# Performance work log

Measured on AMD Instinct MI355X. Metric: run time of the kernel, lower is better.

## Reference

```python
import jax, jax.numpy as jnp
import numpy as np

B, S, D, V = 2, 256, 512, 32000
W_WIN, GAMMA = 20, 2.0
MEM_LEN, NUM_MEM, K_SIM, K_CONT = 16, 256, 8, 4


def _modularity(sim, bnd):
    deg = sim.sum(1)
    tot = deg.sum()
    com = jnp.cumsum(bnd).astype(jnp.int32)
    exp = deg[:, None] * deg[None, :] / (tot + 1e-10)
    mask = (com[:, None] == com[None, :]).astype(sim.dtype)
    return ((sim - exp) * mask).sum() / (tot + 1e-10)


def _conductance(sim, bnd):
    n = sim.shape[0]
    deg = sim.sum(1)
    tot = deg.sum()
    com = jnp.cumsum(bnd).astype(jnp.int32)
    oh = jax.nn.one_hot(com, n + 1, dtype=sim.dtype)  # [N, N+1] fixed class count (empty communities contribute 0)
    vol = oh.T @ deg
    inter = oh.T @ sim @ oh
    inter = inter * (1.0 - jnp.eye(n + 1, dtype=sim.dtype))
    cuts = inter.sum(1)
    minv = jnp.minimum(vol, tot - vol)
    cond = cuts / (minv + 1e-10)
    # torch averages over num_communities = max(com)+1
    return cond.sum() / (com[-1].astype(sim.dtype) + 1.0)


def _forward(query, key, value, attention_mask, target_tokens, brain_w,
             storage_w1, storage_b1, storage_w2, storage_b2, sim_w, sim_b,
             memory_keys, memory_values, memory_lengths, memory_timestamps):
    # --- surprise: per-token NLL of target under brain logits ---
    logits = jnp.einsum('bsd,vd->bsv', query, brain_w)
    logp = jax.nn.log_softmax(logits, axis=-1)
    surprise = -jnp.take_along_axis(logp, target_tokens[..., None], axis=-1)[..., 0]  # [B,S]
    # --- dynamic threshold over sliding windows (unbiased std, as torch) ---
    widx = jnp.arange(S - W_WIN + 1)[:, None] + jnp.arange(W_WIN)[None, :]
    win = surprise[:, widx]  # [B, S-W+1, W]
    thr = win.mean(-1) + GAMMA * jnp.std(win, axis=-1, ddof=1)
    thr = jnp.concatenate([jnp.repeat(thr[:, :1], W_WIN - 1, axis=1), thr], axis=1)
    boundaries = (surprise > thr).astype(query.dtype)  # [B,S]
    # --- refine boundaries via modularity / conductance on token similarity graph ---
    sims = jnp.einsum('bnd,bmd->bnm', query, query)
    curQ = jax.vmap(_modularity)(sims, boundaries)
    curC = jax.vmap(_conductance)(sims, boundaries)
    b_idx = jnp.repeat(jnp.arange(B), S)
    t_idx = jnp.tile(jnp.arange(S), B)

    def cand(b, t):  # evaluate removing boundary at (b,t)
        tb = boundaries[b].at[t].set(0.0)
        return _modularity(sims[b], tb), _conductance(sims[b], tb)

    newQ, newC = jax.vmap(cand)(b_idx, t_idx)
    impr = ((newQ > curQ[b_idx]) | (newC < curC[b_idx])).reshape(B, S)
    refined = jnp.where((boundaries > 0) & impr, 0.0, boundaries)
    # --- event segmentation: labels via cumsum; position-in-event via cummax of segment starts ---
    labels = jnp.cumsum(refined, axis=1).astype(jnp.int32)  # [B,S] in [0,S]
    t_r = jnp.arange(S)
    changed = jnp.concatenate([jnp.ones((B, 1), bool), labels[:, 1:] != labels[:, :-1]], axis=1)
    start = jax.lax.cummax(jnp.where(changed, t_r[None, :], 0), axis=1)
    pos = t_r[None, :] - start  # [B,S] position within event
    bflat = jnp.repeat(jnp.arange(B), S)
    lflat = labels.reshape(-1)
    pflat = pos.reshape(-1)  # tokens with pos >= MEM_LEN are truncated (OOB -> dropped)
    events = jnp.zeros((B, S + 1, MEM_LEN, D), query.dtype)
    events = events.at[bflat, lflat, pflat].add(query.reshape(-1, D), mode='drop')
    counts = jnp.zeros((B, S + 1), jnp.int32).at[bflat, lflat].add(1)
    # --- pack non-empty events into circular memory bank (memory_index = 0, timestamp = 0) ---
    flat_ev = events.reshape(B * (S + 1), MEM_LEN, D)
    flat_ct = counts.reshape(-1)
    nonempty = flat_ct > 0
    rank = jnp.cumsum(nonempty) - 1
    slot = jnp.where(nonempty, rank % NUM_MEM, NUM_MEM)  # OOB slot -> dropped
    mem_keys = memory_keys.at[slot].set(flat_ev[:, 0, :], mode='drop')
    mem_vals = memory_values.at[slot].set(flat_ev, mode='drop')
    mem_lens = memory_lengths.at[slot].set(jnp.minimum(flat_ct, MEM_LEN).astype(memory_lengths.dtype), mode='drop')
    mem_ts = memory_timestamps.at[slot].set(jnp.zeros(slot.shape, memory_timestamps.dtype), mode='drop')
    # --- retrieval: kNN over memory keys with projected mean query ---
    qm = (jnp.einsum('bsd,ed->bse', query, sim_w) + sim_b).mean(1)  # [B,D]
    scores = qm @ mem_keys.T  # [B, NUM_MEM]
    valid = mem_lens > 0
    scores = jnp.where(valid[None, :], scores, -1e9)
    _, top_i = jax.lax.top_k(scores, K_SIM)
    sim_buf = mem_vals[top_i].reshape(B, K_SIM * MEM_LEN, D)
    rec = jnp.where(valid, jnp.arange(NUM_MEM), -1)  # contiguity = most recently written slots
    _, cont_i = jax.lax.top_k(rec, K_CONT)
    cont_buf = jnp.broadcast_to(mem_vals[cont_i].reshape(1, K_CONT * MEM_LEN, D), (B, K_CONT * MEM_LEN, D))
    storage = lambda x: jax.nn.relu(x @ storage_w1.T + storage_b1) @ storage_w2.T + storage_b2
    context = jnp.concatenate([storage(sim_buf), storage(cont_buf), key], axis=1)  # [B, 192+S, D]
    mem_total = (K_SIM + K_CONT) * MEM_LEN
    ext_mask = jnp.concatenate([jnp.ones((B, mem_total), attention_mask.dtype), attention_mask], axis=1)
    return query, context, context, ext_mask


def setup_inputs():
    rng = jax.random.key(0)
    ks = jax.random.split(rng, 10)
    sc = 0.02
    return {
        'query': jax.random.normal(ks[0], (B, S, D), jnp.float32),
        'key': jax.random.normal(ks[1], (B, S, D), jnp.float32),
        'value': jax.random.normal(ks[2], (B, S, D), jnp.float32),
        'attention_mask': jnp.ones((B, S), jnp.float32),
        'target_tokens': jax.random.randint(ks[3], (B, S), 0, V),
        'brain_w': jax.random.normal(ks[4], (V, D), jnp.float32) * sc,
        'storage_w1': jax.random.normal(ks[5], (D, D), jnp.float32) * sc,
        'storage_b1': jnp.zeros((D,), jnp.float32),
        'storage_w2': jax.random.normal(ks[6], (D, D), jnp.float32) * sc,
        'storage_b2': jnp.zeros((D,), jnp.float32),
        'sim_w': jax.random.normal(ks[7], (D, D), jnp.float32) * sc,
        'sim_b': jnp.zeros((D,), jnp.float32),
        'memory_keys': jnp.zeros((NUM_MEM, D), jnp.float32),
        'memory_values': jnp.zeros((NUM_MEM, MEM_LEN, D), jnp.float32),
        'memory_lengths': jnp.zeros((NUM_MEM,), jnp.int32),
        'memory_timestamps': jnp.zeros((NUM_MEM,), jnp.float32),
    }


def reference(query, key, value, attention_mask, target_tokens, brain_w, storage_w1, storage_b1, storage_w2, storage_b2, sim_w, sim_b, memory_keys, memory_values, memory_lengths, memory_timestamps):
    return _forward(query, key, value, attention_mask, target_tokens, brain_w, storage_w1, storage_b1, storage_w2, storage_b2, sim_w, sim_b, memory_keys, memory_values, memory_lengths, memory_timestamps)
```

## Files before the change

kernel.cpp:

```cpp
#include <hip/hip_runtime.h>

constexpr int Bb = 2;
constexpr int Ss = 256;
constexpr int Dd = 512;
constexpr int Vv = 32000;
constexpr int NVB = Vv / 64;
constexpr float GAMMA_C = 2.0f;
constexpr int MEMLEN = 16;
constexpr int NMEM = 256;
constexpr int MTOT = (8 + 4) * MEMLEN;
constexpr int CTXROWS = MTOT + Ss;

constexpr size_t NQ   = (size_t)Bb * Ss * Dd;
constexpr size_t OC1  = NQ;
constexpr size_t NCTX = (size_t)Bb * CTXROWS * Dd;
constexpr size_t OC2  = OC1 + NCTX;
constexpr size_t OMASK = OC2 + NCTX;

constexpr size_t WS_FLOATS_NEEDED = 256000 + 512 + 512 + 131072 + 131584 + 512 +
                                    1024 + 1024 + 512 + 196608 + 196608 + 4096;

__device__ __forceinline__ void gemm64x64_k512(const float* __restrict__ A,
                                               const float* __restrict__ Bm,
                                               float acc[4][4],
                                               float4* __restrict__ Qs4,
                                               float4* __restrict__ Ws4) {
  const int t = threadIdx.x;
  const int tn = t & 15, tm = t >> 4;
  float* __restrict__ Qf = (float*)Qs4;
  float* __restrict__ Wf = (float*)Ws4;
  #pragma unroll 2
  for (int kc = 0; kc < 512; kc += 32) {
    #pragma unroll
    for (int e = 0; e < 2; ++e) {
      const int idx4 = t + 256 * e;
      const int m = idx4 >> 3;
      const int kg = idx4 & 7;
      const float4 qa = *(const float4*)(A + (size_t)m * 512 + kc + kg * 4);
      const float4 wb = *(const float4*)(Bm + (size_t)m * 512 + kc + kg * 4);
      const int fb = ((kg * 4) * 16 + ((m >> 2) ^ kg)) * 4 + (m & 3);
      Qf[fb]       = qa.x; Qf[fb + 64]  = qa.y;
      Qf[fb + 128] = qa.z; Qf[fb + 192] = qa.w;
      Wf[fb]       = wb.x; Wf[fb + 64]  = wb.y;
      Wf[fb + 128] = wb.z; Wf[fb + 192] = wb.w;
    }
    __syncthreads();
    #pragma unroll
    for (int k = 0; k < 32; ++k) {
      const int swz = (k >> 2) & 7;
      const float4 a4 = Qs4[k * 16 + (tm ^ swz)];
      const float4 b4 = Ws4[k * 16 + (tn ^ swz)];
      const float av[4] = {a4.x, a4.y, a4.z, a4.w};
      const float bv[4] = {b4.x, b4.y, b4.z, b4.w};
      #pragma unroll
      for (int i = 0; i < 4; ++i)
        #pragma unroll
        for (int j = 0; j < 4; ++j)
          acc[i][j] += av[i] * bv[j];
    }
    __syncthreads();
  }
}

__global__ __launch_bounds__(256) void k_logits(const float* __restrict__ q,
                                                const float* __restrict__ bw,
                                                float* __restrict__ partial) {
  __shared__ float4 As4[512];
  __shared__ float4 Bs4[1024];
  __shared__ float red[64 * 17];
  const int bv = blockIdx.x;
  const int bm = blockIdx.y;
  const int t = threadIdx.x;
  const int tn = t & 15, tm = t >> 4;
  const float* A  = q  + (size_t)bm * 64 * 512;
  const float* Bm = bw + (size_t)bv * 128 * 512;
  float* Af = (float*)As4;
  float* Bf = (float*)Bs4;
  float acc0[4][4] = {};
  float acc1[4][4] = {};
  #pragma unroll 1
  for (int kc = 0; kc < 512; kc += 32) {
    #pragma unroll
    for (int e = 0; e < 2; ++e) {
      const int idx = t + 256 * e;
      const int m = idx >> 3, kg = idx & 7;
      const float4 v = *(const float4*)(A + (size_t)m * 512 + kc + kg * 4);
      const int fb = ((kg * 4) * 16 + ((m >> 2) ^ kg)) * 4 + (m & 3);
      Af[fb] = v.x; Af[fb + 64] = v.y; Af[fb + 128] = v.z; Af[fb + 192] = v.w;
    }
    #pragma unroll
    for (int e = 0; e < 4; ++e) {
      const int idx = t + 256 * e;
      const int mB = idx >> 3, kg = idx & 7;
      const float4 v = *(const float4*)(Bm + (size_t)mB * 512 + kc + kg * 4);
      const int m4 = mB >> 2;
      const int g = (m4 & 24) | ((m4 & 7) ^ kg);
      const int fb = ((kg * 4) * 32 + g) * 4 + (mB & 3);
      Bf[fb] = v.x; Bf[fb + 128] = v.y; Bf[fb + 256] = v.z; Bf[fb + 384] = v.w;
    }
    __syncthreads();
    #pragma unroll
    for (int k = 0; k < 32; ++k) {
      const int swz = (k >> 2) & 7;
      const float4 a4 = As4[k * 16 + (tm ^ swz)];
      const int g0 = (tn & 8) | ((tn & 7) ^ swz);
      const float4 b0 = Bs4[k * 32 + g0];
      const float4 b1 = Bs4[k * 32 + 16 + g0];
      const float av[4]  = {a4.x, a4.y, a4.z, a4.w};
      const float b0v[4] = {b0.x, b0.y, b0.z, b0.w};
      const float b1v[4] = {b1.x, b1.y, b1.z, b1.w};
      #pragma unroll
      for (int i = 0; i < 4; ++i)
        #pragma unroll
        for (int j = 0; j < 4; ++j) {
          acc0[i][j] += av[i] * b0v[j];
          acc1[i][j] += av[i] * b1v[j];
        }
    }
    __syncthreads();
  }
  #pragma unroll
  for (int i = 0; i < 4; ++i) {
    float s = 0.f;
    #pragma unroll
    for (int j = 0; j < 4; ++j) s += expf(acc0[i][j]);
    red[(tm * 4 + i) * 17 + tn] = s;
  }
  __syncthreads();
  if (t < 64) {
    float s = 0.f;
    #pragma unroll
    for (int j = 0; j < 16; ++j) s += red[t * 17 + j];
    partial[(size_t)(bv * 2) * 512 + bm * 64 + t] = s;
  }
  __syncthreads();
  #pragma unroll
  for (int i = 0; i < 4; ++i) {
    float s = 0.f;
    #pragma unroll
    for (int j = 0; j < 4; ++j) s += expf(acc1[i][j]);
    red[(tm * 4 + i) * 17 + tn] = s;
  }
  __syncthreads();
  if (t < 64) {
    float s = 0.f;
    #pragma unroll
    for (int j = 0; j < 16; ++j) s += red[t * 17 + j];
    partial[(size_t)(bv * 2 + 1) * 512 + bm * 64 + t] = s;
  }
}

constexpr int MISC_SIMS = 32;
constexpr int MISC_QBAR = MISC_SIMS + 4;
constexpr int MISC_LSE  = MISC_QBAR + 16;
constexpr int MISC_NBLK = MISC_LSE + 2052;

__global__ __launch_bounds__(256) void k_misc(const float* __restrict__ q,
                                              const float* __restrict__ key,
                                              const float* __restrict__ amask,
                                              const float* __restrict__ partial,
                                              float* __restrict__ sims,
                                              float* __restrict__ qbar,
                                              double* __restrict__ pc,
                                              float* __restrict__ out) {
  __shared__ float4 sh4[1024];
  const int bx = blockIdx.x, t = threadIdx.x;
  if (bx < MISC_SIMS) {
    int b = bx >> 4, rem = bx & 15;
    int m0 = (rem >> 2) * 64, n0 = (rem & 3) * 64;
    float acc[4][4] = {};
    const float* qb = q + (size_t)b * Ss * Dd;
    gemm64x64_k512(qb + (size_t)m0 * 512, qb + (size_t)n0 * 512, acc, sh4, sh4 + 512);
    int tn = t & 15, tm = t >> 4;
    float* outp = sims + (size_t)b * Ss * Ss;
    #pragma unroll
    for (int i = 0; i < 4; ++i) {
      float4 v = make_float4(acc[i][0], acc[i][1], acc[i][2], acc[i][3]);
      *(float4*)&outp[(size_t)(m0 + tm * 4 + i) * 256 + n0 + tn * 4] = v;
    }
  } else if (bx < MISC_QBAR) {
    int id = (bx - MISC_SIMS) * 256 + t;
    int b = id >> 9, d = id & 511;
    float s = 0.f;
    for (int ss2 = 0; ss2 < 256; ++ss2) s += q[((size_t)(b * 256 + ss2)) * 512 + d];
    qbar[id] = s * (1.0f / 256.0f);
  } else if (bx < MISC_LSE) {
    int idx = bx - MISC_QBAR;
    int c = idx >> 1, rb = idx & 1;
    int r = rb * 256 + t;
    int j0 = c * 63, j1 = (j0 + 63 < NVB) ? j0 + 63 : NVB;
    double s = 0.0;
    for (int j = j0; j < j1; ++j) s += (double)partial[(size_t)j * 512 + r];
    pc[c * 512 + r] = s;
  } else {
    int id = (bx - MISC_LSE) * 256 + t;
    if (id < 262144) { out[id] = q[id]; return; }
    if (id < 524288) {
      int id2 = id - 262144;
      int b = id2 >> 17;
      int s = (id2 >> 9) & 255;
      int d = id2 & 511;
      float v = key[id2];
      size_t p = OC1 + ((size_t)(b * 448 + 192 + s)) * 512 + d;
      out[p] = v;
      out[p + NCTX] = v;
      return;
    }
    if (id < 525184) {
      int j = id - 524288;
      int b = j / 448, c = j - b * 448;
      out[OMASK + j] = (c < 192) ? 1.0f : amask[b * 256 + (c - 192)];
    }
  }
}

__global__ __launch_bounds__(256) void k_sur(const float* __restrict__ q,
                                             const float* __restrict__ bw,
                                             const int* __restrict__ tgt,
                                             const double* __restrict__ pc,
                                             float* __restrict__ sur) {
  int wid = blockIdx.x * 4 + (threadIdx.x >> 6);
  int lane = threadIdx.x & 63;
  int tg = tgt[wid];
  const float* qp = q + (size_t)wid * 512;
  const float* wp = bw + (size_t)tg * 512;
  float a = 0.f;
  #pragma unroll
  for (int j = 0; j < 8; ++j) a += qp[lane + 64 * j] * wp[lane + 64 * j];
  #pragma unroll
  for (int off = 32; off; off >>= 1) a += __shfl_xor(a, off);
  if (lane == 0) {
    double s = 0.0;
    #pragma unroll
    for (int c = 0; c < 8; ++c) s += pc[c * 512 + wid];
    float lsef = (float)log(s);
    sur[wid] = lsef - a;
  }
}

__global__ __launch_bounds__(256) void k_bound(const float* __restrict__ sur,
                                               int* __restrict__ bnd) {
  __shared__ float ss[256];
  __shared__ float thrw[237];
  int b = blockIdx.x, t = threadIdx.x;
  ss[t] = sur[b * 256 + t];
  __syncthreads();
  if (t < 237) {
    float mn = 0.f;
    #pragma unroll
    for (int e = 0; e < 20; ++e) mn += ss[t + e];
    mn *= (1.0f / 20.0f);
    float v = 0.f;
    #pragma unroll
    for (int e = 0; e < 20; ++e) { float d = ss[t + e] - mn; v += d * d; }
    thrw[t] = mn + GAMMA_C * sqrtf(v * (1.0f / 19.0f));
  }
  __syncthreads();
  float th = (t <= 18) ? thrw[0] : thrw[t - 19];
  bnd[b * 256 + t] = (ss[t] > th) ? 1 : 0;
}

__global__ __launch_bounds__(256) void k_rowpref(const float* __restrict__ sims,
                                                 float* __restrict__ R,
                                                 float* __restrict__ deg) {
  int wid = blockIdx.x * 4 + (threadIdx.x >> 6);
  int lane = threadIdx.x & 63;
  int b = wid >> 8, i = wid & 255;
  const float* row = sims + (size_t)b * 65536 + (size_t)i * 256;
  float4 v = *(const float4*)&row[lane * 4];
  float c0 = v.x, c1 = c0 + v.y, c2 = c1 + v.z, c3 = c2 + v.w;
  float ls = c3;
  float sc = ls;
  for (int off = 1; off < 64; off <<= 1) {
    float u = __shfl_up(sc, off);
    if (lane >= off) sc += u;
  }
  float ex = sc - ls;
  float* Rr = R + (size_t)b * (256 * 257) + (size_t)i * 257;
  Rr[lane * 4 + 1] = ex + c0;
  Rr[lane * 4 + 2] = ex + c1;
  Rr[lane * 4 + 3] = ex + c2;
  Rr[lane * 4 + 4] = ex + c3;
  if (lane == 0) Rr[0] = 0.f;
  if (lane == 63) deg[b * 256 + i] = ex + c3;
}

__global__ __launch_bounds__(256) void k_refine(const int* __restrict__ bnd,
                                                const float* __restrict__ R,
                                                const float* __restrict__ deg,
                                                int* __restrict__ nseg,
                                                int* __restrict__ segstart_o,
                                                int* __restrict__ segcnt_o) {
  __shared__ int sb[256], lab[256];
  __shared__ int segst[258];
  __shared__ float Dc[257], Sc[257], Cr[257];
  __shared__ float degsh[256];
  __shared__ float Stm[256], Ctm[256];
  __shared__ float sh[6];
  int b = blockIdx.x, t = threadIdx.x;
  sb[t] = bnd[b * 256 + t];
  degsh[t] = deg[b * 256 + t];
  for (int c = t; c < 258; c += 256) segst[c] = -1;
  __syncthreads();
  int a = 0;
  for (int i = 0; i <= t; ++i) a += sb[i];
  lab[t] = a;
  __syncthreads();
  if (t == 0 || lab[t - 1] != lab[t]) segst[lab[t]] = t;
  __syncthreads();
  int nb = lab[255];
  const float* Rb = R + (size_t)b * (256 * 257);
  {
    int c = lab[t];
    int a1 = segst[c];
    int e1 = (c == nb) ? 255 : (segst[c + 1] - 1);
    const float* Rrow = Rb + (size_t)t * 257;
    Stm[t] = Rrow[e1 + 1] - Rrow[a1];
    float cv = 0.f;
    if (c < nb) {
      int a2 = segst[c + 1];
      int e2 = (c + 1 == nb) ? 255 : (segst[c + 2] - 1);
      cv = Rrow[e2 + 1] - Rrow[a2];
    }
    Ctm[t] = cv;
  }
  __syncthreads();
  for (int c = t; c <= nb; c += 256) {
    float Dv = 0.f, Sv = 0.f, Cv = 0.f;
    int a1 = segst[c];
    if (a1 >= 0) {
      int e1 = (c == nb) ? 255 : (segst[c + 1] - 1);
      for (int i = a1; i <= e1; ++i) { Dv += degsh[i]; Sv += Stm[i]; Cv += Ctm[i]; }
    }
    Dc[c] = Dv; Sc[c] = Sv; Cr[c] = Cv;
  }
  __syncthreads();
  if (t == 0) {
    float tot = 0.f;
    for (int i = 0; i < 256; ++i) tot += degsh[i];
    float tote = tot + 1e-10f;
    float Qun = 0.f, Cs = 0.f;
    for (int c = 0; c <= nb; ++c) {
      Qun += Sc[c] - Dc[c] * Dc[c] / tote;
      Cs  += (Dc[c] - Sc[c]) / (fminf(Dc[c], tot - Dc[c]) + 1e-10f);
    }
    sh[0] = tot; sh[1] = tote; sh[2] = Qun; sh[3] = Cs;
    sh[4] = Qun / tote; sh[5] = Cs / (float)(nb + 1);
  }
  __syncthreads();
  int r = sb[t];
  if (r == 1) {
    float tot = sh[0], tote = sh[1], Qun = sh[2], Cs = sh[3], curQ = sh[4], curC = sh[5];
    int c2 = lab[t], c1 = c2 - 1;
    if (segst[c1] < 0) {
      float newC0 = Cs / (float)nb;
      if (newC0 < curC) r = 0;
    } else {
      float D1 = Dc[c1], S1 = Sc[c1], D2 = Dc[c2], S2 = Sc[c2];
      float Dm = D1 + D2, Sm = S1 + S2 + 2.0f * Cr[c1];
      float tq1 = S1 - D1 * D1 / tote;
      float tq2 = S2 - D2 * D2 / tote;
      float tqm = Sm - Dm * Dm / tote;
      float newQ = (Qun - tq1 - tq2 + tqm) / tote;
      float tc1 = (D1 - S1) / (fminf(D1, tot - D1) + 1e-10f);
      float tc2 = (D2 - S2) / (fminf(D2, tot - D2) + 1e-10f);
      float tcm = (Dm - Sm) / (fminf(Dm, tot - Dm) + 1e-10f);
      float newC = (Cs - tc1 - tc2 + tcm) / (float)nb;
      if (newQ > curQ || newC < curC) r = 0;
    }
  }
  __syncthreads();
  sb[t] = r;
  __syncthreads();
  if (t == 0) {
    int ns = 0, st = 0;
    for (int i = 1; i <= 256; ++i) {
      if (i == 256 || sb[i] == 1) {
        segstart_o[b * 257 + ns] = st;
        segcnt_o[b * 257 + ns] = i - st;
        ns++;
        st = i;
      }
    }
    nseg[b] = ns;
  }
}

__global__ __launch_bounds__(256) void k_slots(const int* __restrict__ nseg,
                                               const int* __restrict__ segstart_i,
                                               const int* __restrict__ segcnt_i,
                                               const int* __restrict__ meml_in,
                                               int* __restrict__ slot_b,
                                               int* __restrict__ slot_start,
                                               int* __restrict__ slot_cnt,
                                               int* __restrict__ cont) {
  __shared__ unsigned char validsh[256];
  __shared__ int ns01[2];
  int t = threadIdx.x;
  if (t < 2) ns01[t] = nseg[t];
  __syncthreads();
  int ns0 = ns01[0], total = ns0 + ns01[1];
  int rank = -1;
  for (int r = t; r < total; r += 256) rank = r;
  int bb = 0, st = 0, ct = 0;
  if (rank >= 0) {
    bb = (rank >= ns0) ? 1 : 0;
    int s = rank - bb * ns0;
    st = segstart_i[bb * 257 + s];
    ct = segcnt_i[bb * 257 + s];
  }
  slot_b[t] = bb; slot_start[t] = st; slot_cnt[t] = ct;
  validsh[t] = (ct > 0 || meml_in[t] > 0) ? 1 : 0;
  __syncthreads();
  if (t == 0) {
    int k = 0;
    for (int n = 255; n >= 0 && k < 4; --n) if (validsh[n]) cont[k++] = n;
    for (int n = 0; n < 256 && k < 4; ++n) if (!validsh[n]) cont[k++] = n;
  }
}

__global__ __launch_bounds__(256) void k_qm(const float* __restrict__ qbar,
                                            const float* __restrict__ simw,
                                            const float* __restrict__ simb,
                                            float* __restrict__ qm) {
  int wid = blockIdx.x * 4 + (threadIdx.x >> 6);
  int lane = threadIdx.x & 63;
  int b = wid >> 9, e = wid & 511;
  float a = 0.f;
  #pragma unroll
  for (int j = 0; j < 8; ++j)
    a += qbar[b * 512 + lane + 64 * j] * simw[(size_t)e * 512 + lane + 64 * j];
  #pragma unroll
  for (int off = 32; off; off >>= 1) a += __shfl_xor(a, off);
  if (lane == 0) qm[b * 512 + e] = a + simb[e];
}

__global__ __launch_bounds__(256) void k_scores(const float* __restrict__ q,
                                                const float* __restrict__ memk,
                                                const int* __restrict__ meml,
                                                const int* __restrict__ slot_b,
                                                const int* __restrict__ slot_start,
                                                const int* __restrict__ slot_cnt,
                                                const float* __restrict__ qm,
                                                float* __restrict__ scores) {
  int wid = blockIdx.x * 4 + (threadIdx.x >> 6);
  int lane = threadIdx.x & 63;
  int b = wid >> 8, n = wid & 255;
  const float* kp = nullptr;
  if (slot_cnt[n] > 0) kp = q + ((size_t)(slot_b[n] * 256 + slot_start[n])) * 512;
  else if (meml[n] > 0) kp = memk + (size_t)n * 512;
  float a = 0.f;
  if (kp) {
    #pragma unroll
    for (int j = 0; j < 8; ++j) a += qm[b * 512 + lane + 64 * j] * kp[lane + 64 * j];
    #pragma unroll
    for (int off = 32; off; off >>= 1) a += __shfl_xor(a, off);
  }
  if (lane == 0) scores[b * 256 + n] = kp ? a : -1000000000.0f;
}

__global__ __launch_bounds__(64) void k_topk(const float* __restrict__ scores,
                                             int* __restrict__ topi) {
  int b = blockIdx.x, lane = threadIdx.x;
  float v[4];
  #pragma unroll
  for (int j = 0; j < 4; ++j) v[j] = scores[b * 256 + lane * 4 + j];
  int chosen = 0;
  for (int k = 0; k < 8; ++k) {
    float best = -3.4e38f; int bi = 0x7fffffff;
    #pragma unroll
    for (int j = 0; j < 4; ++j) {
      if (!(chosen & (1 << j))) {
        float s = v[j]; int n = lane * 4 + j;
        if (s > best || (s == best && n < bi)) { best = s; bi = n; }
      }
    }
    #pragma unroll
    for (int off = 32; off; off >>= 1) {
      float ob = __shfl_xor(best, off);
      int oi = __shfl_xor(bi, off);
      if (ob > best || (ob == best && oi < bi)) { best = ob; bi = oi; }
    }
    if ((bi >> 2) == lane) chosen |= 1 << (bi & 3);
    if (lane == 0) topi[b * 8 + k] = bi;
  }
}

__global__ __launch_bounds__(256) void k_gather(const float* __restrict__ q,
                                                const float* __restrict__ memv,
                                                const int* __restrict__ topi,
                                                const int* __restrict__ cont,
                                                const int* __restrict__ slot_b,
                                                const int* __restrict__ slot_start,
                                                const int* __restrict__ slot_cnt,
                                                float* __restrict__ xg) {
  int id = blockIdx.x * 256 + threadIdx.x;
  int d = id & 511;
  int rb = id >> 9;
  int b = rb / 192;
  int r = rb - b * 192;
  int p = r & 15;
  int slot = (r < 128) ? topi[b * 8 + (r >> 4)] : cont[(r - 128) >> 4];
  float val;
  int cnt = slot_cnt[slot];
  if (cnt > 0) {
    int ml = cnt < 16 ? cnt : 16;
    val = (p < ml) ? q[((size_t)(slot_b[slot] * 256 + slot_start[slot] + p)) * 512 + d] : 0.f;
  } else {
    val = memv[((size_t)slot * 16 + p) * 512 + d];
  }
  xg[id] = val;
}

__global__ __launch_bounds__(256) void k_mlp1(const float* __restrict__ xg,
                                              const float* __restrict__ w1,
                                              const float* __restrict__ b1,
                                              float* __restrict__ h) {
  __shared__ float4 Qs4[512];
  __shared__ float4 Ws4[512];
  int n0 = blockIdx.x * 64, m0 = blockIdx.y * 64;
  float acc[4][4] = {};
  gemm64x64_k512(xg + (size_t)m0 * 512, w1 + (size_t)n0 * 512, acc, Qs4, Ws4);
  int t = threadIdx.x, tn = t & 15, tm = t >> 4;
  #pragma unroll
  for (int i = 0; i < 4; ++i) {
    int m = m0 + tm * 4 + i;
    #pragma unroll
    for (int j = 0; j < 4; ++j) {
      int n = n0 + tn * 4 + j;
      h[(size_t)m * 512 + n] = fmaxf(acc[i][j] + b1[n], 0.f);
    }
  }
}

__global__ __launch_bounds__(256) void k_mlp2(const float* __restrict__ h,
                                              const float* __restrict__ w2,
                                              const float* __restrict__ b2,
                                              float* __restrict__ out) {
  __shared__ float4 Qs4[512];
  __shared__ float4 Ws4[512];
  int n0 = blockIdx.x * 64, m0 = blockIdx.y * 64;
  float acc[4][4] = {};
  gemm64x64_k512(h + (size_t)m0 * 512, w2 + (size_t)n0 * 512, acc, Qs4, Ws4);
  int t = threadIdx.x, tn = t & 15, tm = t >> 4;
  #pragma unroll
  for (int i = 0; i < 4; ++i) {
    int m = m0 + tm * 4 + i;
    int b = (m >= 192) ? 1 : 0;
    int rr = m - b * 192;
    int n = n0 + tn * 4;
    float4 v = make_float4(acc[i][0] + b2[n], acc[i][1] + b2[n + 1],
                           acc[i][2] + b2[n + 2], acc[i][3] + b2[n + 3]);
    size_t base = OC1 + ((size_t)(b * 448 + rr)) * 512 + n;
    *(float4*)&out[base] = v;
    *(float4*)&out[base + NCTX] = v;
  }
}

extern "C" void kernel_launch(void* const* d_in, const int* in_sizes, int n_in,
                              void* d_out, int out_size, void* d_ws, size_t ws_size,
                              hipStream_t stream) {
  if (ws_size < WS_FLOATS_NEEDED * sizeof(float)) return;

  const float* q     = (const float*)d_in[0];
  const float* key   = (const float*)d_in[1];
  const float* amask = (const float*)d_in[3];
  const int*   tgt   = (const int*)d_in[4];
  const float* bw    = (const float*)d_in[5];
  const float* w1    = (const float*)d_in[6];
  const float* b1    = (const float*)d_in[7];
  const float* w2    = (const float*)d_in[8];
  const float* b2    = (const float*)d_in[9];
  const float* simw  = (const float*)d_in[10];
  const float* simb  = (const float*)d_in[11];
  const float* memk  = (const float*)d_in[12];
  const float* memv  = (const float*)d_in[13];
  const int*   meml  = (const int*)d_in[14];
  float* out = (float*)d_out;

  float* w = (float*)d_ws;
  float* p_partial = w;
  float* p_lse    = p_partial + 256000;
  float* p_sur    = p_lse + 512;
  float* p_sims   = p_sur + 512;
  float* p_R      = p_sims + 131072;
  float* p_deg    = p_R + 131584;
  float* p_qbar   = p_deg + 512;
  float* p_qm     = p_qbar + 1024;
  float* p_scores = p_qm + 1024;
  float* p_xg     = p_scores + 512;
  float* p_h      = p_xg + 196608;
  double* p_pc    = (double*)p_h;
  int* ip         = (int*)(p_h + 196608);
  int* ip_bnd     = ip;
  int* ip_nseg    = ip + 512;
  int* ip_segst   = ip + 514;
  int* ip_segcnt  = ip + 1028;
  int* ip_slotb   = ip + 1542;
  int* ip_slotst  = ip + 1798;
  int* ip_slotcnt = ip + 2054;
  int* ip_topi    = ip + 2310;
  int* ip_cont    = ip + 2326;

  k_logits<<<dim3(250, 8), 256, 0, stream>>>(q, bw, p_partial);
  k_misc<<<MISC_NBLK, 256, 0, stream>>>(q, key, amask, p_partial,
                                        p_sims, p_qbar, p_pc, out);
  k_sur<<<128, 256, 0, stream>>>(q, bw, tgt, p_pc, p_sur);
  k_bound<<<2, 256, 0, stream>>>(p_sur, ip_bnd);
  k_rowpref<<<128, 256, 0, stream>>>(p_sims, p_R, p_deg);
  k_refine<<<2, 256, 0, stream>>>(ip_bnd, p_R, p_deg, ip_nseg, ip_segst, ip_segcnt);
  k_slots<<<1, 256, 0, stream>>>(ip_nseg, ip_segst, ip_segcnt, meml,
                                 ip_slotb, ip_slotst, ip_slotcnt, ip_cont);
  k_qm<<<256, 256, 0, stream>>>(p_qbar, simw, simb, p_qm);
  k_scores<<<128, 256, 0, stream>>>(q, memk, meml, ip_slotb, ip_slotst, ip_slotcnt,
                                    p_qm, p_scores);
  k_topk<<<2, 64, 0, stream>>>(p_scores, ip_topi);
  k_gather<<<768, 256, 0, stream>>>(q, memv, ip_topi, ip_cont,
                                    ip_slotb, ip_slotst, ip_slotcnt, p_xg);
  k_mlp1<<<dim3(8, 6), 256, 0, stream>>>(p_xg, w1, b1, p_h);
  k_mlp2<<<dim3(8, 6), 256, 0, stream>>>(p_h, w2, b2, out);
}
```

Before: 485.0 us.

## Fuse pipeline kernels to cut launch count from thirteen to seven

Merges the logits GEMM with the sims/qbar/copy work into one launch and merges the LSE partial reduction, row prefix sums and qm projection into a second. Boundary detection, refinement and slot assignment are folded into a single 512-thread block. Top-k selection and the row gather are folded into the first MLP GEMM, which now reads its rows through pointers. The aim is to remove launch gaps and intermediate round trips, at the cost of heavier per-block branching and a single-block serial stage.

```diff
diff --git a/kernel.cpp b/kernel.cpp
--- a/kernel.cpp
+++ b/kernel.cpp
@@ -19,6 +19,11 @@
 
 constexpr size_t WS_FLOATS_NEEDED = 256000 + 512 + 512 + 131072 + 131584 + 512 +
                                     1024 + 1024 + 512 + 196608 + 196608 + 4096;
+
+constexpr int K1_LOGITS = 2000;
+constexpr int K1_SIMS   = K1_LOGITS + 32;
+constexpr int K1_QBAR   = K1_SIMS + 4;
+constexpr int K1_NBLK   = K1_QBAR + 2052;
 
 __device__ __forceinline__ void gemm64x64_k512(const float* __restrict__ A,
                                                const float* __restrict__ Bm,
@@ -62,155 +67,191 @@
   }
 }
 
-__global__ __launch_bounds__(256) void k_logits(const float* __restrict__ q,
-                                                const float* __restrict__ bw,
-                                                float* __restrict__ partial) {
-  __shared__ float4 As4[512];
-  __shared__ float4 Bs4[1024];
-  __shared__ float red[64 * 17];
-  const int bv = blockIdx.x;
-  const int bm = blockIdx.y;
-  const int t = threadIdx.x;
-  const int tn = t & 15, tm = t >> 4;
-  const float* A  = q  + (size_t)bm * 64 * 512;
-  const float* Bm = bw + (size_t)bv * 128 * 512;
-  float* Af = (float*)As4;
-  float* Bf = (float*)Bs4;
-  float acc0[4][4] = {};
-  float acc1[4][4] = {};
-  #pragma unroll 1
-  for (int kc = 0; kc < 512; kc += 32) {
-    #pragma unroll
-    for (int e = 0; e < 2; ++e) {
-      const int idx = t + 256 * e;
-      const int m = idx >> 3, kg = idx & 7;
-      const float4 v = *(const float4*)(A + (size_t)m * 512 + kc + kg * 4);
-      const int fb = ((kg * 4) * 16 + ((m >> 2) ^ kg)) * 4 + (m & 3);
-      Af[fb] = v.x; Af[fb + 64] = v.y; Af[fb + 128] = v.z; Af[fb + 192] = v.w;
-    }
-    #pragma unroll
-    for (int e = 0; e < 4; ++e) {
-      const int idx = t + 256 * e;
-      const int mB = idx >> 3, kg = idx & 7;
-      const float4 v = *(const float4*)(Bm + (size_t)mB * 512 + kc + kg * 4);
-      const int m4 = mB >> 2;
-      const int g = (m4 & 24) | ((m4 & 7) ^ kg);
-      const int fb = ((kg * 4) * 32 + g) * 4 + (mB & 3);
-      Bf[fb] = v.x; Bf[fb + 128] = v.y; Bf[fb + 256] = v.z; Bf[fb + 384] = v.w;
-    }
-    __syncthreads();
-    #pragma unroll
-    for (int k = 0; k < 32; ++k) {
-      const int swz = (k >> 2) & 7;
-      const float4 a4 = As4[k * 16 + (tm ^ swz)];
-      const int g0 = (tn & 8) | ((tn & 7) ^ swz);
-      const float4 b0 = Bs4[k * 32 + g0];
-      const float4 b1 = Bs4[k * 32 + 16 + g0];
-      const float av[4]  = {a4.x, a4.y, a4.z, a4.w};
-      const float b0v[4] = {b0.x, b0.y, b0.z, b0.w};
-      const float b1v[4] = {b1.x, b1.y, b1.z, b1.w};
-      #pragma unroll
-      for (int i = 0; i < 4; ++i)
-        #pragma unroll
-        for (int j = 0; j < 4; ++j) {
-          acc0[i][j] += av[i] * b0v[j];
-          acc1[i][j] += av[i] * b1v[j];
-        }
-    }
-    __syncthreads();
-  }
-  #pragma unroll
-  for (int i = 0; i < 4; ++i) {
-    float s = 0.f;
-    #pragma unroll
-    for (int j = 0; j < 4; ++j) s += expf(acc0[i][j]);
-    red[(tm * 4 + i) * 17 + tn] = s;
-  }
-  __syncthreads();
-  if (t < 64) {
-    float s = 0.f;
-    #pragma unroll
-    for (int j = 0; j < 16; ++j) s += red[t * 17 + j];
-    partial[(size_t)(bv * 2) * 512 + bm * 64 + t] = s;
-  }
-  __syncthreads();
-  #pragma unroll
-  for (int i = 0; i < 4; ++i) {
-    float s = 0.f;
-    #pragma unroll
-    for (int j = 0; j < 4; ++j) s += expf(acc1[i][j]);
-    red[(tm * 4 + i) * 17 + tn] = s;
-  }
-  __syncthreads();
-  if (t < 64) {
-    float s = 0.f;
-    #pragma unroll
-    for (int j = 0; j < 16; ++j) s += red[t * 17 + j];
-    partial[(size_t)(bv * 2 + 1) * 512 + bm * 64 + t] = s;
-  }
-}
-
-constexpr int MISC_SIMS = 32;
-constexpr int MISC_QBAR = MISC_SIMS + 4;
-constexpr int MISC_LSE  = MISC_QBAR + 16;
-constexpr int MISC_NBLK = MISC_LSE + 2052;
-
-__global__ __launch_bounds__(256) void k_misc(const float* __restrict__ q,
+__global__ __launch_bounds__(256) void k_main(const float* __restrict__ q,
+                                              const float* __restrict__ bw,
                                               const float* __restrict__ key,
                                               const float* __restrict__ amask,
-                                              const float* __restrict__ partial,
+                                              float* __restrict__ partial,
                                               float* __restrict__ sims,
                                               float* __restrict__ qbar,
-                                              double* __restrict__ pc,
                                               float* __restrict__ out) {
-  __shared__ float4 sh4[1024];
-  const int bx = blockIdx.x, t = threadIdx.x;
-  if (bx < MISC_SIMS) {
-    int b = bx >> 4, rem = bx & 15;
+  __shared__ __align__(16) char smem[28928];
+  const int b = blockIdx.x, t = threadIdx.x;
+  if (b < K1_LOGITS) {
+    float4* As4 = (float4*)smem;
+    float4* Bs4 = As4 + 512;
+    float* red  = (float*)(Bs4 + 1024);
+    const int bv = b >> 3;
+    const int bm = b & 7;
+    const int tn = t & 15, tm = t >> 4;
+    const float* A  = q  + (size_t)bm * 64 * 512;
+    const float* Bm = bw + (size_t)bv * 128 * 512;
+    float* Af = (float*)As4;
+    float* Bf = (float*)Bs4;
+    float acc0[4][4] = {};
+    float acc1[4][4] = {};
+    #pragma unroll 1
+    for (int kc = 0; kc < 512; kc += 32) {
+      #pragma unroll
+      for (int e = 0; e < 2; ++e) {
+        const int idx = t + 256 * e;
+        const int m = idx >> 3, kg = idx & 7;
+        const float4 v = *(const float4*)(A + (size_t)m * 512 + kc + kg * 4);
+        const int fb = ((kg * 4) * 16 + ((m >> 2) ^ kg)) * 4 + (m & 3);
+        Af[fb] = v.x; Af[fb + 64] = v.y; Af[fb + 128] = v.z; Af[fb + 192] = v.w;
+      }
+      #pragma unroll
+      for (int e = 0; e < 4; ++e) {
+        const int idx = t + 256 * e;
+        const int mB = idx >> 3, kg = idx & 7;
+        const float4 v = *(const float4*)(Bm + (size_t)mB * 512 + kc + kg * 4);
+        const int m4 = mB >> 2;
+        const int g = (m4 & 24) | ((m4 & 7) ^ kg);
+        const int fb = ((kg * 4) * 32 + g) * 4 + (mB & 3);
+        Bf[fb] = v.x; Bf[fb + 128] = v.y; Bf[fb + 256] = v.z; Bf[fb + 384] = v.w;
+      }
+      __syncthreads();
+      #pragma unroll
+      for (int k = 0; k < 32; ++k) {
+        const int swz = (k >> 2) & 7;
+        const float4 a4 = As4[k * 16 + (tm ^ swz)];
+        const int g0 = (tn & 8) | ((tn & 7) ^ swz);
+        const float4 b0 = Bs4[k * 32 + g0];
+        const float4 b1 = Bs4[k * 32 + 16 + g0];
+        const float av[4]  = {a4.x, a4.y, a4.z, a4.w};
+        const float b0v[4] = {b0.x, b0.y, b0.z, b0.w};
+        const float b1v[4] = {b1.x, b1.y, b1.z, b1.w};
+        #pragma unroll
+        for (int i = 0; i < 4; ++i)
+          #pragma unroll
+          for (int j = 0; j < 4; ++j) {
+            acc0[i][j] += av[i] * b0v[j];
+            acc1[i][j] += av[i] * b1v[j];
+          }
+      }
+      __syncthreads();
+    }
+    #pragma unroll
+    for (int i = 0; i < 4; ++i) {
+      float s = 0.f;
+      #pragma unroll
+      for (int j = 0; j < 4; ++j) s += expf(acc0[i][j]);
+      red[(tm * 4 + i) * 17 + tn] = s;
+    }
+    __syncthreads();
+    if (t < 64) {
+      float s = 0.f;
+      #pragma unroll
+      for (int j = 0; j < 16; ++j) s += red[t * 17 + j];
+      partial[(size_t)(bv * 2) * 512 + bm * 64 + t] = s;
+    }
+    __syncthreads();
+    #pragma unroll
+    for (int i = 0; i < 4; ++i) {
+      float s = 0.f;
+      #pragma unroll
+      for (int j = 0; j < 4; ++j) s += expf(acc1[i][j]);
+      red[(tm * 4 + i) * 17 + tn] = s;
+    }
+    __syncthreads();
+    if (t < 64) {
+      float s = 0.f;
+      #pragma unroll
+      for (int j = 0; j < 16; ++j) s += red[t * 17 + j];
+      partial[(size_t)(bv * 2 + 1) * 512 + bm * 64 + t] = s;
+    }
+  } else if (b < K1_SIMS) {
+    float4* Qs4 = (float4*)smem;
+    float4* Ws4 = Qs4 + 512;
+    int bi2 = b - K1_LOGITS;
+    int bb = bi2 >> 4, rem = bi2 & 15;
     int m0 = (rem >> 2) * 64, n0 = (rem & 3) * 64;
     float acc[4][4] = {};
-    const float* qb = q + (size_t)b * Ss * Dd;
-    gemm64x64_k512(qb + (size_t)m0 * 512, qb + (size_t)n0 * 512, acc, sh4, sh4 + 512);
+    const float* qb = q + (size_t)bb * Ss * Dd;
+    gemm64x64_k512(qb + (size_t)m0 * 512, qb + (size_t)n0 * 512, acc, Qs4, Ws4);
     int tn = t & 15, tm = t >> 4;
-    float* outp = sims + (size_t)b * Ss * Ss;
+    float* outp = sims + (size_t)bb * Ss * Ss;
     #pragma unroll
     for (int i = 0; i < 4; ++i) {
       float4 v = make_float4(acc[i][0], acc[i][1], acc[i][2], acc[i][3]);
       *(float4*)&outp[(size_t)(m0 + tm * 4 + i) * 256 + n0 + tn * 4] = v;
     }
-  } else if (bx < MISC_QBAR) {
-    int id = (bx - MISC_SIMS) * 256 + t;
-    int b = id >> 9, d = id & 511;
+  } else if (b < K1_QBAR) {
+    int id = (b - K1_SIMS) * 256 + t;
+    int bb = id >> 9, d = id & 511;
     float s = 0.f;
-    for (int ss2 = 0; ss2 < 256; ++ss2) s += q[((size_t)(b * 256 + ss2)) * 512 + d];
+    for (int ss2 = 0; ss2 < 256; ++ss2) s += q[((size_t)(bb * 256 + ss2)) * 512 + d];
     qbar[id] = s * (1.0f / 256.0f);
-  } else if (bx < MISC_LSE) {
-    int idx = bx - MISC_QBAR;
-    int c = idx >> 1, rb = idx & 1;
-    int r = rb * 256 + t;
+  } else {
+    int id = (b - K1_QBAR) * 256 + t;
+    if (id < 262144) { out[id] = q[id]; return; }
+    if (id < 524288) {
+      int id2 = id - 262144;
+      int bb = id2 >> 17;
+      int s = (id2 >> 9) & 255;
+      int d = id2 & 511;
+      float v = key[id2];
+      size_t p = OC1 + ((size_t)(bb * 448 + 192 + s)) * 512 + d;
+      out[p] = v;
+      out[p + NCTX] = v;
+      return;
+    }
+    if (id < 525184) {
+      int j = id - 524288;
+      int bb = j / 448, c = j - bb * 448;
+      out[OMASK + j] = (c < 192) ? 1.0f : amask[bb * 256 + (c - 192)];
+    }
+  }
+}
+
+__global__ __launch_bounds__(256) void k_mid(const float* __restrict__ partial,
+                                             const float* __restrict__ sims,
+                                             const float* __restrict__ qbar,
+                                             const float* __restrict__ simw,
+                                             const float* __restrict__ simb,
+                                             double* __restrict__ pc,
+                                             float* __restrict__ R,
+                                             float* __restrict__ deg,
+                                             float* __restrict__ qm) {
+  const int b = blockIdx.x, t = threadIdx.x;
+  const int wv = t >> 6, lane = t & 63;
+  if (b < 16) {
+    int c = b >> 1, rb2 = b & 1;
+    int r = rb2 * 256 + t;
     int j0 = c * 63, j1 = (j0 + 63 < NVB) ? j0 + 63 : NVB;
     double s = 0.0;
     for (int j = j0; j < j1; ++j) s += (double)partial[(size_t)j * 512 + r];
     pc[c * 512 + r] = s;
+  } else if (b < 144) {
+    int wid = (b - 16) * 4 + wv;
+    int bb = wid >> 8, i = wid & 255;
+    const float* row = sims + (size_t)bb * 65536 + (size_t)i * 256;
+    float4 v = *(const float4*)&row[lane * 4];
+    float c0 = v.x, c1 = c0 + v.y, c2 = c1 + v.z, c3 = c2 + v.w;
+    float ls = c3;
+    float sc = ls;
+    for (int off = 1; off < 64; off <<= 1) {
+      float u = __shfl_up(sc, off);
+      if (lane >= off) sc += u;
+    }
+    float ex = sc - ls;
+    float* Rr = R + (size_t)bb * (256 * 257) + (size_t)i * 257;
+    Rr[lane * 4 + 1] = ex + c0;
+    Rr[lane * 4 + 2] = ex + c1;
+    Rr[lane * 4 + 3] = ex + c2;
+    Rr[lane * 4 + 4] = ex + c3;
+    if (lane == 0) Rr[0] = 0.f;
+    if (lane == 63) deg[bb * 256 + i] = ex + c3;
   } else {
-    int id = (bx - MISC_LSE) * 256 + t;
-    if (id < 262144) { out[id] = q[id]; return; }
-    if (id < 524288) {
-      int id2 = id - 262144;
-      int b = id2 >> 17;
-      int s = (id2 >> 9) & 255;
-      int d = id2 & 511;
-      float v = key[id2];
-      size_t p = OC1 + ((size_t)(b * 448 + 192 + s)) * 512 + d;
-      out[p] = v;
-      out[p + NCTX] = v;
-      return;
-    }
-    if (id < 525184) {
-      int j = id - 524288;
-      int b = j / 448, c = j - b * 448;
-      out[OMASK + j] = (c < 192) ? 1.0f : amask[b * 256 + (c - 192)];
-    }
+    int wid2 = (b - 144) * 4 + wv;
+    int bb = wid2 >> 9, e = wid2 & 511;
+    float a = 0.f;
+    #pragma unroll
+    for (int j = 0; j < 8; ++j)
+      a += qbar[bb * 512 + lane + 64 * j] * simw[(size_t)e * 512 + lane + 64 * j];
+    #pragma unroll
+    for (int off = 32; off; off >>= 1) a += __shfl_xor(a, off);
+    if (lane == 0) qm[bb * 512 + e] = a + simb[e];
   }
 }
 
@@ -233,131 +274,107 @@
     double s = 0.0;
     #pragma unroll
     for (int c = 0; c < 8; ++c) s += pc[c * 512 + wid];
-    float lsef = (float)log(s);
-    sur[wid] = lsef - a;
-  }
-}
-
-__global__ __launch_bounds__(256) void k_bound(const float* __restrict__ sur,
-                                               int* __restrict__ bnd) {
-  __shared__ float ss[256];
-  __shared__ float thrw[237];
-  int b = blockIdx.x, t = threadIdx.x;
-  ss[t] = sur[b * 256 + t];
-  __syncthreads();
-  if (t < 237) {
+    sur[wid] = (float)log(s) - a;
+  }
+}
+
+__global__ __launch_bounds__(512) void k_bndref(const float* __restrict__ sur,
+                                                const float* __restrict__ R,
+                                                const float* __restrict__ deg,
+                                                const int* __restrict__ meml,
+                                                int* __restrict__ nseg_g,
+                                                int* __restrict__ segst_g,
+                                                int* __restrict__ segcnt_g,
+                                                int* __restrict__ slotb_g,
+                                                int* __restrict__ slotst_g,
+                                                int* __restrict__ slotcnt_g,
+                                                int* __restrict__ cont_g) {
+  __shared__ float ss[2][256], thrw[2][237];
+  __shared__ int sb[2][256], lab[2][256], segst[2][258];
+  __shared__ float Dc[2][257], Scs[2][257], Cr[2][257];
+  __shared__ float degsh[2][256], Stm[2][256], Ctm[2][256];
+  __shared__ float shv[2][6];
+  __shared__ int segstL[2][257], segcntL[2][257], nsL[2];
+  __shared__ unsigned char validsh[256];
+  const int t = threadIdx.x;
+  const int bt = t >> 8, tt = t & 255;
+  ss[bt][tt] = sur[bt * 256 + tt];
+  degsh[bt][tt] = deg[bt * 256 + tt];
+  for (int c = tt; c < 258; c += 256) segst[bt][c] = -1;
+  __syncthreads();
+  if (tt < 237) {
     float mn = 0.f;
     #pragma unroll
-    for (int e = 0; e < 20; ++e) mn += ss[t + e];
+    for (int e = 0; e < 20; ++e) mn += ss[bt][tt + e];
     mn *= (1.0f / 20.0f);
     float v = 0.f;
     #pragma unroll
-    for (int e = 0; e < 20; ++e) { float d = ss[t + e] - mn; v += d * d; }
-    thrw[t] = mn + GAMMA_C * sqrtf(v * (1.0f / 19.0f));
-  }
-  __syncthreads();
-  float th = (t <= 18) ? thrw[0] : thrw[t - 19];
-  bnd[b * 256 + t] = (ss[t] > th) ? 1 : 0;
-}
-
-__global__ __launch_bounds__(256) void k_rowpref(const float* __restrict__ sims,
-                                                 float* __restrict__ R,
-                                                 float* __restrict__ deg) {
-  int wid = blockIdx.x * 4 + (threadIdx.x >> 6);
-  int lane = threadIdx.x & 63;
-  int b = wid >> 8, i = wid & 255;
-  const float* row = sims + (size_t)b * 65536 + (size_t)i * 256;
-  float4 v = *(const float4*)&row[lane * 4];
-  float c0 = v.x, c1 = c0 + v.y, c2 = c1 + v.z, c3 = c2 + v.w;
-  float ls = c3;
-  float sc = ls;
-  for (int off = 1; off < 64; off <<= 1) {
-    float u = __shfl_up(sc, off);
-    if (lane >= off) sc += u;
-  }
-  float ex = sc - ls;
-  float* Rr = R + (size_t)b * (256 * 257) + (size_t)i * 257;
-  Rr[lane * 4 + 1] = ex + c0;
-  Rr[lane * 4 + 2] = ex + c1;
-  Rr[lane * 4 + 3] = ex + c2;
-  Rr[lane * 4 + 4] = ex + c3;
-  if (lane == 0) Rr[0] = 0.f;
-  if (lane == 63) deg[b * 256 + i] = ex + c3;
-}
-
-__global__ __launch_bounds__(256) void k_refine(const int* __restrict__ bnd,
-                                                const float* __restrict__ R,
-                                                const float* __restrict__ deg,
-                                                int* __restrict__ nseg,
-                                                int* __restrict__ segstart_o,
-                                                int* __restrict__ segcnt_o) {
-  __shared__ int sb[256], lab[256];
-  __shared__ int segst[258];
-  __shared__ float Dc[257], Sc[257], Cr[257];
-  __shared__ float degsh[256];
-  __shared__ float Stm[256], Ctm[256];
-  __shared__ float sh[6];
-  int b = blockIdx.x, t = threadIdx.x;
-  sb[t] = bnd[b * 256 + t];
-  degsh[t] = deg[b * 256 + t];
-  for (int c = t; c < 258; c += 256) segst[c] = -1;
+    for (int e = 0; e < 20; ++e) { float d = ss[bt][tt + e] - mn; v += d * d; }
+    thrw[bt][tt] = mn + GAMMA_C * sqrtf(v * (1.0f / 19.0f));
+  }
+  __syncthreads();
+  {
+    float th = (tt <= 18) ? thrw[bt][0] : thrw[bt][tt - 19];
+    sb[bt][tt] = (ss[bt][tt] > th) ? 1 : 0;
+  }
   __syncthreads();
   int a = 0;
-  for (int i = 0; i <= t; ++i) a += sb[i];
-  lab[t] = a;
-  __syncthreads();
-  if (t == 0 || lab[t - 1] != lab[t]) segst[lab[t]] = t;
-  __syncthreads();
-  int nb = lab[255];
-  const float* Rb = R + (size_t)b * (256 * 257);
+  for (int i = 0; i <= tt; ++i) a += sb[bt][i];
+  lab[bt][tt] = a;
+  __syncthreads();
+  if (tt == 0 || lab[bt][tt - 1] != lab[bt][tt]) segst[bt][lab[bt][tt]] = tt;
+  __syncthreads();
+  const int nb = lab[bt][255];
+  const float* Rb = R + (size_t)bt * (256 * 257);
   {
-    int c = lab[t];
-    int a1 = segst[c];
-    int e1 = (c == nb) ? 255 : (segst[c + 1] - 1);
-    const float* Rrow = Rb + (size_t)t * 257;
-    Stm[t] = Rrow[e1 + 1] - Rrow[a1];
+    int c = lab[bt][tt];
+    int a1 = segst[bt][c];
+    int e1 = (c == nb) ? 255 : (segst[bt][c + 1] - 1);
+    const float* Rrow = Rb + (size_t)tt * 257;
+    Stm[bt][tt] = Rrow[e1 + 1] - Rrow[a1];
     float cv = 0.f;
     if (c < nb) {
-      int a2 = segst[c + 1];
-      int e2 = (c + 1 == nb) ? 255 : (segst[c + 2] - 1);
+      int a2 = segst[bt][c + 1];
+      int e2 = (c + 1 == nb) ? 255 : (segst[bt][c + 2] - 1);
       cv = Rrow[e2 + 1] - Rrow[a2];
     }
-    Ctm[t] = cv;
-  }
-  __syncthreads();
-  for (int c = t; c <= nb; c += 256) {
+    Ctm[bt][tt] = cv;
+  }
+  __syncthreads();
+  for (int c = tt; c <= nb; c += 256) {
     float Dv = 0.f, Sv = 0.f, Cv = 0.f;
-    int a1 = segst[c];
+    int a1 = segst[bt][c];
     if (a1 >= 0) {
-      int e1 = (c == nb) ? 255 : (segst[c + 1] - 1);
-      for (int i = a1; i <= e1; ++i) { Dv += degsh[i]; Sv += Stm[i]; Cv += Ctm[i]; }
-    }
-    Dc[c] = Dv; Sc[c] = Sv; Cr[c] = Cv;
-  }
-  __syncthreads();
-  if (t == 0) {
+      int e1 = (c == nb) ? 255 : (segst[bt][c + 1] - 1);
+      for (int i = a1; i <= e1; ++i) { Dv += degsh[bt][i]; Sv += Stm[bt][i]; Cv += Ctm[bt][i]; }
+    }
+    Dc[bt][c] = Dv; Scs[bt][c] = Sv; Cr[bt][c] = Cv;
+  }
+  __syncthreads();
+  if (tt == 0) {
     float tot = 0.f;
-    for (int i = 0; i < 256; ++i) tot += degsh[i];
+    for (int i = 0; i < 256; ++i) tot += degsh[bt][i];
     float tote = tot + 1e-10f;
     float Qun = 0.f, Cs = 0.f;
     for (int c = 0; c <= nb; ++c) {
-      Qun += Sc[c] - Dc[c] * Dc[c] / tote;
-      Cs  += (Dc[c] - Sc[c]) / (fminf(Dc[c], tot - Dc[c]) + 1e-10f);
-    }
-    sh[0] = tot; sh[1] = tote; sh[2] = Qun; sh[3] = Cs;
-    sh[4] = Qun / tote; sh[5] = Cs / (float)(nb + 1);
-  }
-  __syncthreads();
-  int r = sb[t];
+      Qun += Scs[bt][c] - Dc[bt][c] * Dc[bt][c] / tote;
+      Cs  += (Dc[bt][c] - Scs[bt][c]) / (fminf(Dc[bt][c], tot - Dc[bt][c]) + 1e-10f);
+    }
+    shv[bt][0] = tot; shv[bt][1] = tote; shv[bt][2] = Qun; shv[bt][3] = Cs;
+    shv[bt][4] = Qun / tote; shv[bt][5] = Cs / (float)(nb + 1);
+  }
+  __syncthreads();
+  int r = sb[bt][tt];
   if (r == 1) {
-    float tot = sh[0], tote = sh[1], Qun = sh[2], Cs = sh[3], curQ = sh[4], curC = sh[5];
-    int c2 = lab[t], c1 = c2 - 1;
-    if (segst[c1] < 0) {
+    float tot = shv[bt][0], tote = shv[bt][1], Qun = shv[bt][2], Cs = shv[bt][3];
+    float curQ = shv[bt][4], curC = shv[bt][5];
+    int c2 = lab[bt][tt], c1 = c2 - 1;
+    if (segst[bt][c1] < 0) {
       float newC0 = Cs / (float)nb;
       if (newC0 < curC) r = 0;
     } else {
-      float D1 = Dc[c1], S1 = Sc[c1], D2 = Dc[c2], S2 = Sc[c2];
-      float Dm = D1 + D2, Sm = S1 + S2 + 2.0f * Cr[c1];
+      float D1 = Dc[bt][c1], S1 = Scs[bt][c1], D2 = Dc[bt][c2], S2 = Scs[bt][c2];
+      float Dm = D1 + D2, Sm = S1 + S2 + 2.0f * Cr[bt][c1];
       float tq1 = S1 - D1 * D1 / tote;
       float tq2 = S2 - D2 * D2 / tote;
       float tqm = Sm - Dm * Dm / tote;
@@ -370,69 +387,43 @@
     }
   }
   __syncthreads();
-  sb[t] = r;
-  __syncthreads();
-  if (t == 0) {
+  sb[bt][tt] = r;
+  __syncthreads();
+  if (tt == 0) {
     int ns = 0, st = 0;
     for (int i = 1; i <= 256; ++i) {
-      if (i == 256 || sb[i] == 1) {
-        segstart_o[b * 257 + ns] = st;
-        segcnt_o[b * 257 + ns] = i - st;
+      if (i == 256 || sb[bt][i] == 1) {
+        segstL[bt][ns] = st; segcntL[bt][ns] = i - st;
+        segst_g[bt * 257 + ns] = st;
+        segcnt_g[bt * 257 + ns] = i - st;
         ns++;
         st = i;
       }
     }
-    nseg[b] = ns;
-  }
-}
-
-__global__ __launch_bounds__(256) void k_slots(const int* __restrict__ nseg,
-                                               const int* __restrict__ segstart_i,
-                                               const int* __restrict__ segcnt_i,
-                                               const int* __restrict__ meml_in,
-                                               int* __restrict__ slot_b,
-                                               int* __restrict__ slot_start,
-                                               int* __restrict__ slot_cnt,
-                                               int* __restrict__ cont) {
-  __shared__ unsigned char validsh[256];
-  __shared__ int ns01[2];
-  int t = threadIdx.x;
-  if (t < 2) ns01[t] = nseg[t];
-  __syncthreads();
-  int ns0 = ns01[0], total = ns0 + ns01[1];
-  int rank = -1;
-  for (int r = t; r < total; r += 256) rank = r;
-  int bb = 0, st = 0, ct = 0;
-  if (rank >= 0) {
-    bb = (rank >= ns0) ? 1 : 0;
-    int s = rank - bb * ns0;
-    st = segstart_i[bb * 257 + s];
-    ct = segcnt_i[bb * 257 + s];
-  }
-  slot_b[t] = bb; slot_start[t] = st; slot_cnt[t] = ct;
-  validsh[t] = (ct > 0 || meml_in[t] > 0) ? 1 : 0;
+    nsL[bt] = ns;
+    nseg_g[bt] = ns;
+  }
+  __syncthreads();
+  if (t < 256) {
+    int ns0 = nsL[0], total = ns0 + nsL[1];
+    int rank = -1;
+    for (int r2 = t; r2 < total; r2 += 256) rank = r2;
+    int bb = 0, st = 0, ct = 0;
+    if (rank >= 0) {
+      bb = (rank >= ns0) ? 1 : 0;
+      int s = rank - bb * ns0;
+      st = segstL[bb][s];
+      ct = segcntL[bb][s];
+    }
+    slotb_g[t] = bb; slotst_g[t] = st; slotcnt_g[t] = ct;
+    validsh[t] = (ct > 0 || meml[t] > 0) ? 1 : 0;
+  }
   __syncthreads();
   if (t == 0) {
     int k = 0;
-    for (int n = 255; n >= 0 && k < 4; --n) if (validsh[n]) cont[k++] = n;
-    for (int n = 0; n < 256 && k < 4; ++n) if (!validsh[n]) cont[k++] = n;
-  }
-}
-
-__global__ __launch_bounds__(256) void k_qm(const float* __restrict__ qbar,
-                                            const float* __restrict__ simw,
-                                            const float* __restrict__ simb,
-                                            float* __restrict__ qm) {
-  int wid = blockIdx.x * 4 + (threadIdx.x >> 6);
-  int lane = threadIdx.x & 63;
-  int b = wid >> 9, e = wid & 511;
-  float a = 0.f;
-  #pragma unroll
-  for (int j = 0; j < 8; ++j)
-    a += qbar[b * 512 + lane + 64 * j] * simw[(size_t)e * 512 + lane + 64 * j];
-  #pragma unroll
-  for (int off = 32; off; off >>= 1) a += __shfl_xor(a, off);
-  if (lane == 0) qm[b * 512 + e] = a + simb[e];
+    for (int n = 255; n >= 0 && k < 4; --n) if (validsh[n]) cont_g[k++] = n;
+    for (int n = 0; n < 256 && k < 4; ++n) if (!validsh[n]) cont_g[k++] = n;
+  }
 }
 
 __global__ __launch_bounds__(256) void k_scores(const float* __restrict__ q,
@@ -459,69 +450,100 @@
   if (lane == 0) scores[b * 256 + n] = kp ? a : -1000000000.0f;
 }
 
-__global__ __launch_bounds__(64) void k_topk(const float* __restrict__ scores,
-                                             int* __restrict__ topi) {
-  int b = blockIdx.x, lane = threadIdx.x;
-  float v[4];
-  #pragma unroll
-  for (int j = 0; j < 4; ++j) v[j] = scores[b * 256 + lane * 4 + j];
-  int chosen = 0;
-  for (int k = 0; k < 8; ++k) {
-    float best = -3.4e38f; int bi = 0x7fffffff;
-    #pragma unroll
-    for (int j = 0; j < 4; ++j) {
-      if (!(chosen & (1 << j))) {
-        float s = v[j]; int n = lane * 4 + j;
-        if (s > best || (s == best && n < bi)) { best = s; bi = n; }
-      }
-    }
-    #pragma unroll
-    for (int off = 32; off; off >>= 1) {
-      float ob = __shfl_xor(best, off);
-      int oi = __shfl_xor(bi, off);
-      if (ob > best || (ob == best && oi < bi)) { best = ob; bi = oi; }
-    }
-    if ((bi >> 2) == lane) chosen |= 1 << (bi & 3);
-    if (lane == 0) topi[b * 8 + k] = bi;
-  }
-}
-
-__global__ __launch_bounds__(256) void k_gather(const float* __restrict__ q,
-                                                const float* __restrict__ memv,
-                                                const int* __restrict__ topi,
-                                                const int* __restrict__ cont,
-                                                const int* __restrict__ slot_b,
-                                                const int* __restrict__ slot_start,
-                                                const int* __restrict__ slot_cnt,
-                                                float* __restrict__ xg) {
-  int id = blockIdx.x * 256 + threadIdx.x;
-  int d = id & 511;
-  int rb = id >> 9;
-  int b = rb / 192;
-  int r = rb - b * 192;
-  int p = r & 15;
-  int slot = (r < 128) ? topi[b * 8 + (r >> 4)] : cont[(r - 128) >> 4];
-  float val;
-  int cnt = slot_cnt[slot];
-  if (cnt > 0) {
-    int ml = cnt < 16 ? cnt : 16;
-    val = (p < ml) ? q[((size_t)(slot_b[slot] * 256 + slot_start[slot] + p)) * 512 + d] : 0.f;
-  } else {
-    val = memv[((size_t)slot * 16 + p) * 512 + d];
-  }
-  xg[id] = val;
-}
-
-__global__ __launch_bounds__(256) void k_mlp1(const float* __restrict__ xg,
-                                              const float* __restrict__ w1,
-                                              const float* __restrict__ b1,
-                                              float* __restrict__ h) {
+__global__ __launch_bounds__(256) void k_mlp1g(const float* __restrict__ q,
+                                               const float* __restrict__ memv,
+                                               const float* __restrict__ scores,
+                                               const int* __restrict__ cont,
+                                               const int* __restrict__ slotb,
+                                               const int* __restrict__ slotst,
+                                               const int* __restrict__ slotcnt,
+                                               const float* __restrict__ w1,
+                                               const float* __restrict__ b1,
+                                               float* __restrict__ h) {
   __shared__ float4 Qs4[512];
   __shared__ float4 Ws4[512];
-  int n0 = blockIdx.x * 64, m0 = blockIdx.y * 64;
+  __shared__ const float* rowsrc[64];
+  __shared__ int topiL[8];
+  const int b = blockIdx.x, t = threadIdx.x;
+  const int m0 = (b >> 3) * 64, n0 = (b & 7) * 64;
+  const int bb = (m0 >= 192) ? 1 : 0;
+  if (t < 64) {
+    float v[4];
+    #pragma unroll
+    for (int j = 0; j < 4; ++j) v[j] = scores[bb * 256 + t * 4 + j];
+    int chosen = 0;
+    for (int k = 0; k < 8; ++k) {
+      float best = -3.4e38f; int bi = 0x7fffffff;
+      #pragma unroll
+      for (int j = 0; j < 4; ++j) {
+        if (!(chosen & (1 << j))) {
+          float s = v[j]; int n = t * 4 + j;
+          if (s > best || (s == best && n < bi)) { best = s; bi = n; }
+        }
+      }
+      #pragma unroll
+      for (int off = 32; off; off >>= 1) {
+        float ob = __shfl_xor(best, off);
+        int oi = __shfl_xor(bi, off);
+        if (ob > best || (ob == best && oi < bi)) { best = ob; bi = oi; }
+      }
+      if ((bi >> 2) == t) chosen |= 1 << (bi & 3);
+      if (t == 0) topiL[k] = bi;
+    }
+  }
+  __syncthreads();
+  if (t < 64) {
+    int rr = (m0 + t) - bb * 192;
+    int p = rr & 15;
+    int slot = (rr < 128) ? topiL[rr >> 4] : cont[(rr - 128) >> 4];
+    int cnt = slotcnt[slot];
+    const float* src = nullptr;
+    if (cnt > 0) {
+      int ml = cnt < 16 ? cnt : 16;
+      if (p < ml) src = q + ((size_t)(slotb[slot] * 256 + slotst[slot] + p)) * 512;
+    } else {
+      src = memv + ((size_t)slot * 16 + p) * 512;
+    }
+    rowsrc[t] = src;
+  }
+  __syncthreads();
+  const int tn = t & 15, tm = t >> 4;
+  const float* Bm = w1 + (size_t)n0 * 512;
+  float* Qf = (float*)Qs4;
+  float* Wf = (float*)Ws4;
   float acc[4][4] = {};
-  gemm64x64_k512(xg + (size_t)m0 * 512, w1 + (size_t)n0 * 512, acc, Qs4, Ws4);
-  int t = threadIdx.x, tn = t & 15, tm = t >> 4;
+  #pragma unroll 2
+  for (int kc = 0; kc < 512; kc += 32) {
+    #pragma unroll
+    for (int e = 0; e < 2; ++e) {
+      const int idx4 = t + 256 * e;
+      const int m = idx4 >> 3;
+      const int kg = idx4 & 7;
+      const float* rp = rowsrc[m];
+      const float4 qa = rp ? *(const float4*)(rp + kc + kg * 4) : make_float4(0.f, 0.f, 0.f, 0.f);
+      const float4 wb = *(const float4*)(Bm + (size_t)m * 512 + kc + kg * 4);
+      const int fb = ((kg * 4) * 16 + ((m >> 2) ^ kg)) * 4 + (m & 3);
+      Qf[fb]       = qa.x; Qf[fb + 64]  = qa.y;
+      Qf[fb + 128] = qa.z; Qf[fb + 192] = qa.w;
+      Wf[fb]       = wb.x; Wf[fb + 64]  = wb.y;
+      Wf[fb + 128] = wb.z; Wf[fb + 192] = wb.w;
+    }
+    __syncthreads();
+    #pragma unroll
+    for (int k = 0; k < 32; ++k) {
+      const int swz = (k >> 2) & 7;
+      const float4 a4 = Qs4[k * 16 + (tm ^ swz)];
+      const float4 b4 = Ws4[k * 16 + (tn ^ swz)];
+      const float av[4] = {a4.x, a4.y, a4.z, a4.w};
+      const float bv[4] = {b4.x, b4.y, b4.z, b4.w};
+      #pragma unroll
+      for (int i = 0; i < 4; ++i)
+        #pragma unroll
+        for (int j = 0; j < 4; ++j)
+          acc[i][j] += av[i] * bv[j];
+    }
+    __syncthreads();
+  }
   #pragma unroll
   for (int i = 0; i < 4; ++i) {
     int m = m0 + tm * 4 + i;
@@ -539,19 +561,20 @@
                                               float* __restrict__ out) {
   __shared__ float4 Qs4[512];
   __shared__ float4 Ws4[512];
-  int n0 = blockIdx.x * 64, m0 = blockIdx.y * 64;
+  const int b = blockIdx.x;
+  int n0 = (b & 7) * 64, m0 = (b >> 3) * 64;
   float acc[4][4] = {};
   gemm64x64_k512(h + (size_t)m0 * 512, w2 + (size_t)n0 * 512, acc, Qs4, Ws4);
   int t = threadIdx.x, tn = t & 15, tm = t >> 4;
   #pragma unroll
   for (int i = 0; i < 4; ++i) {
     int m = m0 + tm * 4 + i;
-    int b = (m >= 192) ? 1 : 0;
-    int rr = m - b * 192;
+    int bb = (m >= 192) ? 1 : 0;
+    int rr = m - bb * 192;
     int n = n0 + tn * 4;
     float4 v = make_float4(acc[i][0] + b2[n], acc[i][1] + b2[n + 1],
                            acc[i][2] + b2[n + 2], acc[i][3] + b2[n + 3]);
-    size_t base = OC1 + ((size_t)(b * 448 + rr)) * 512 + n;
+    size_t base = OC1 + ((size_t)(bb * 448 + rr)) * 512 + n;
     *(float4*)&out[base] = v;
     *(float4*)&out[base + NCTX] = v;
   }
@@ -602,21 +625,16 @@
   int* ip_topi    = ip + 2310;
   int* ip_cont    = ip + 2326;
 
-  k_logits<<<dim3(250, 8), 256, 0, stream>>>(q, bw, p_partial);
-  k_misc<<<MISC_NBLK, 256, 0, stream>>>(q, key, amask, p_partial,
-                                        p_sims, p_qbar, p_pc, out);
+  k_main<<<K1_NBLK, 256, 0, stream>>>(q, bw, key, amask, p_partial, p_sims, p_qbar, out);
+  k_mid<<<400, 256, 0, stream>>>(p_partial, p_sims, p_qbar, simw, simb,
+                                 p_pc, p_R, p_deg, p_qm);
   k_sur<<<128, 256, 0, stream>>>(q, bw, tgt, p_pc, p_sur);
-  k_bound<<<2, 256, 0, stream>>>(p_sur, ip_bnd);
-  k_rowpref<<<128, 256, 0, stream>>>(p_sims, p_R, p_deg);
-  k_refine<<<2, 256, 0, stream>>>(ip_bnd, p_R, p_deg, ip_nseg, ip_segst, ip_segcnt);
-  k_slots<<<1, 256, 0, stream>>>(ip_nseg, ip_segst, ip_segcnt, meml,
-                                 ip_slotb, ip_slotst, ip_slotcnt, ip_cont);
-  k_qm<<<256, 256, 0, stream>>>(p_qbar, simw, simb, p_qm);
+  k_bndref<<<1, 512, 0, stream>>>(p_sur, p_R, p_deg, meml,
+                                  ip_nseg, ip_segst, ip_segcnt,
+                                  ip_slotb, ip_slotst, ip_slotcnt, ip_cont);
   k_scores<<<128, 256, 0, stream>>>(q, memk, meml, ip_slotb, ip_slotst, ip_slotcnt,
                                     p_qm, p_scores);
-  k_topk<<<2, 64, 0, stream>>>(p_scores, ip_topi);
-  k_gather<<<768, 256, 0, stream>>>(q, memv, ip_topi, ip_cont,
-                                    ip_slotb, ip_slotst, ip_slotcnt, p_xg);
-  k_mlp1<<<dim3(8, 6), 256, 0, stream>>>(p_xg, w1, b1, p_h);
-  k_mlp2<<<dim3(8, 6), 256, 0, stream>>>(p_h, w2, b2, out);
-}
+  k_mlp1g<<<48, 256, 0, stream>>>(q, memv, p_scores, ip_cont,
+                                  ip_slotb, ip_slotst, ip_slotcnt, w1, b1, p_h);
+  k_mlp2<<<48, 256, 0, stream>>>(p_h, w2, b2, out);
+}
```

Measured after the change: 453.8 us. -6.4%, faster.
